# Optimization experiments

Measured on AMD Instinct MI355X. Metric: run time of the kernel, lower is better.

## Reference

```python
import jax, jax.numpy as jnp
import numpy as np

OMEGA = 10.0
SIGMA = 10.0
HID = 256
IN_DIM = 3
OUT_DIM = 3


def gabor(x, W, b):
    # torch.nn.Linear: lin = x @ W.T + b
    lin = x @ W.T + b
    # exp(1j*omega*lin - (sigma*lin)**2).real == cos(omega*lin) * exp(-(sigma*lin)**2)
    return jnp.cos(OMEGA * lin) * jnp.exp(-jnp.square(SIGMA * lin))


def _linear_init(key, out_dim, in_dim):
    kw, kb = jax.random.split(key)
    bound = 1.0 / np.sqrt(in_dim)
    W = jax.random.uniform(kw, (out_dim, in_dim), jnp.float32, -bound, bound)
    b = jax.random.uniform(kb, (out_dim,), jnp.float32, -bound, bound)
    return W, b


def setup_inputs() -> dict:
    key = jax.random.key(0)
    keys = jax.random.split(key, 7)
    N = 262144
    x = jax.random.uniform(keys[0], (N, IN_DIM), jnp.float32)
    W0, b0 = _linear_init(keys[1], HID, IN_DIM)
    W1, b1 = _linear_init(keys[2], HID, HID)
    W2, b2 = _linear_init(keys[3], HID, HID)
    W3, b3 = _linear_init(keys[4], HID, HID + IN_DIM)  # skip-concat layer
    W4, b4 = _linear_init(keys[5], HID, HID)
    Wf, bf = _linear_init(keys[6], OUT_DIM, HID)
    return {"x": x, "W0": W0, "b0": b0, "W1": W1, "b1": b1, "W2": W2,
            "b2": b2, "W3": W3, "b3": b3, "W4": W4, "b4": b4,
            "Wf": Wf, "bf": bf}


def reference(x, W0, b0, W1, b1, W2, b2, W3, b3, W4, b4, Wf, bf):
    x_in = x
    h = gabor(x, W0, b0)          # net[0]
    h = gabor(h, W1, b1)          # net[1]
    h = gabor(h, W2, b2)          # net[2]
    h = jnp.concatenate([h, x_in], axis=-1)  # skip before net[3]
    h = gabor(h, W3, b3)          # net[3]
    h = gabor(h, W4, b4)          # net[4]
    return h @ Wf.T + bf          # final linear
```

## Files before the change

### kernel.cpp

```cpp
#include <hip/hip_runtime.h>

typedef _Float16 f16x8 __attribute__((ext_vector_type(8)));
typedef _Float16 f16x4 __attribute__((ext_vector_type(4)));
typedef float    f32x4 __attribute__((ext_vector_type(4)));

#define BN    64
#define KPAD  288
#define ROWB  (KPAD * 2)
#define WELE  270336

__device__ __forceinline__ int swz(int row, int colb) {
  int c = (colb < 512) ? (colb ^ ((row & 7) << 4)) : colb;
  return row * ROWB + c;
}

__device__ __forceinline__ float gabor_f(float lin) {
  float a = 10.f * lin;
  return __cosf(a) * __expf(-a * a);
}

template <int KS>
__device__ __forceinline__ void mfma_layer(const char* __restrict__ inb,
                                           char* __restrict__ outb,
                                           const _Float16* __restrict__ Wh,
                                           const _Float16* __restrict__ Wl,
                                           const float* __restrict__ bias,
                                           int lane, int wid) {
  const int r = lane & 15;
  const int g = lane >> 4;
  const int n0 = wid * 32;
  const int x = (r & 7) << 4;

  int boff[4][2];
#pragma unroll
  for (int j = 0; j < 4; j++) {
    const int row = j * 16 + r;
    boff[j][0] = row * ROWB + ((g * 16) ^ x);
    boff[j][1] = row * ROWB + ((64 + g * 16) ^ x);
  }

  f32x4 acc[2][4];
#pragma unroll
  for (int i = 0; i < 2; i++)
#pragma unroll
    for (int j = 0; j < 4; j++) {
      f32x4 z = {0.f, 0.f, 0.f, 0.f};
      acc[i][j] = z;
    }

  const int wbase = (wid * KS) * 1024 + lane * 8;

#pragma unroll
  for (int kk = 0; kk < KS; kk++) {
    const int wof = wbase + kk * 1024;
    f16x8 a0 = *(const f16x8*)(Wh + wof);
    f16x8 a1 = *(const f16x8*)(Wh + wof + 512);
    f16x8 c0 = *(const f16x8*)(Wl + wof);
    f16x8 c1 = *(const f16x8*)(Wl + wof + 512);

    f16x8 b0, b1, b2, b3;
    if (kk < 8) {
      const int imm = (kk >> 1) * 128;
      b0 = *(const f16x8*)(inb + boff[0][kk & 1] + imm);
      b1 = *(const f16x8*)(inb + boff[1][kk & 1] + imm);
      b2 = *(const f16x8*)(inb + boff[2][kk & 1] + imm);
      b3 = *(const f16x8*)(inb + boff[3][kk & 1] + imm);
    } else {
      const int lin0 = r * ROWB + 512 + g * 16;
      b0 = *(const f16x8*)(inb + lin0);
      b1 = *(const f16x8*)(inb + lin0 + 16 * ROWB);
      b2 = *(const f16x8*)(inb + lin0 + 32 * ROWB);
      b3 = *(const f16x8*)(inb + lin0 + 48 * ROWB);
    }

    acc[0][0] = __builtin_amdgcn_mfma_f32_16x16x32_f16(a0, b0, acc[0][0], 0, 0, 0);
    acc[0][1] = __builtin_amdgcn_mfma_f32_16x16x32_f16(a0, b1, acc[0][1], 0, 0, 0);
    acc[0][2] = __builtin_amdgcn_mfma_f32_16x16x32_f16(a0, b2, acc[0][2], 0, 0, 0);
    acc[0][3] = __builtin_amdgcn_mfma_f32_16x16x32_f16(a0, b3, acc[0][3], 0, 0, 0);
    acc[1][0] = __builtin_amdgcn_mfma_f32_16x16x32_f16(a1, b0, acc[1][0], 0, 0, 0);
    acc[1][1] = __builtin_amdgcn_mfma_f32_16x16x32_f16(a1, b1, acc[1][1], 0, 0, 0);
    acc[1][2] = __builtin_amdgcn_mfma_f32_16x16x32_f16(a1, b2, acc[1][2], 0, 0, 0);
    acc[1][3] = __builtin_amdgcn_mfma_f32_16x16x32_f16(a1, b3, acc[1][3], 0, 0, 0);
    acc[0][0] = __builtin_amdgcn_mfma_f32_16x16x32_f16(c0, b0, acc[0][0], 0, 0, 0);
    acc[0][1] = __builtin_amdgcn_mfma_f32_16x16x32_f16(c0, b1, acc[0][1], 0, 0, 0);
    acc[0][2] = __builtin_amdgcn_mfma_f32_16x16x32_f16(c0, b2, acc[0][2], 0, 0, 0);
    acc[0][3] = __builtin_amdgcn_mfma_f32_16x16x32_f16(c0, b3, acc[0][3], 0, 0, 0);
    acc[1][0] = __builtin_amdgcn_mfma_f32_16x16x32_f16(c1, b0, acc[1][0], 0, 0, 0);
    acc[1][1] = __builtin_amdgcn_mfma_f32_16x16x32_f16(c1, b1, acc[1][1], 0, 0, 0);
    acc[1][2] = __builtin_amdgcn_mfma_f32_16x16x32_f16(c1, b2, acc[1][2], 0, 0, 0);
    acc[1][3] = __builtin_amdgcn_mfma_f32_16x16x32_f16(c1, b3, acc[1][3], 0, 0, 0);
  }

#pragma unroll
  for (int i = 0; i < 2; i++) {
    const f32x4 bv = *(const f32x4*)(bias + n0 + i * 16 + g * 4);
#pragma unroll
    for (int j = 0; j < 4; j++) {
      f16x4 hv;
#pragma unroll
      for (int e = 0; e < 4; e++)
        hv[e] = (_Float16)gabor_f(acc[i][j][e] + bv[e]);
      *(f16x4*)(outb + swz(j * 16 + r, (n0 + i * 16 + g * 4) * 2)) = hv;
    }
  }
}

extern "C" __global__ void __launch_bounds__(512, 3)
inr_fused(const float* __restrict__ x, const float* __restrict__ W0,
          const float* __restrict__ b0, const float* __restrict__ b1,
          const float* __restrict__ b2, const float* __restrict__ b3,
          const float* __restrict__ b4, const float* __restrict__ Wf,
          const float* __restrict__ bf, const _Float16* __restrict__ wsh,
          float* __restrict__ out, int npts) {
  extern __shared__ char smem[];
  char* bufA = smem;
  char* bufB = smem + BN * ROWB;

  const _Float16* w1h = wsh;
  const _Float16* w2h = wsh + 65536;
  const _Float16* w4h = wsh + 131072;
  const _Float16* w3p = wsh + 196608;
  const _Float16* w1l = wsh + WELE;
  const _Float16* w2l = wsh + WELE + 65536;
  const _Float16* w4l = wsh + WELE + 131072;
  const _Float16* w3l = wsh + WELE + 196608;

  const int tid   = threadIdx.x;
  const int pbase = blockIdx.x * BN;

  {
    const int p = tid >> 3;
    const int q = tid & 7;
    const int gp = pbase + p;
    float x0 = 0.f, x1 = 0.f, x2 = 0.f;
    if (gp < npts) {
      x0 = x[(size_t)gp * 3 + 0];
      x1 = x[(size_t)gp * 3 + 1];
      x2 = x[(size_t)gp * 3 + 2];
    }
#pragma unroll
    for (int ub = 0; ub < 32; ub += 8) {
      const int u0 = q * 32 + ub;
      f16x8 hv;
#pragma unroll
      for (int e = 0; e < 8; e++) {
        const int u = u0 + e;
        float lin = fmaf(x0, W0[u * 3 + 0],
                    fmaf(x1, W0[u * 3 + 1],
                    fmaf(x2, W0[u * 3 + 2], b0[u])));
        hv[e] = (_Float16)gabor_f(lin);
      }
      *(f16x8*)(bufA + swz(p, u0 * 2)) = hv;
    }
    if (q < 4) {
      f16x8 xv = {(_Float16)0.f, (_Float16)0.f, (_Float16)0.f, (_Float16)0.f,
                  (_Float16)0.f, (_Float16)0.f, (_Float16)0.f, (_Float16)0.f};
      if (q == 0) { xv[0] = (_Float16)x0; xv[1] = (_Float16)x1; xv[2] = (_Float16)x2; }
      *(f16x8*)(bufA + swz(p, (256 + q * 8) * 2)) = xv;
    }
  }
  __syncthreads();

  const int lane = tid & 63;
  const int wid  = tid >> 6;

  mfma_layer<8>(bufA, bufB, w1h, w1l, b1, lane, wid);
  __syncthreads();
  mfma_layer<8>(bufB, bufA, w2h, w2l, b2, lane, wid);
  __syncthreads();
  mfma_layer<9>(bufA, bufB, w3p, w3l, b3, lane, wid);
  __syncthreads();
  mfma_layer<8>(bufB, bufA, w4h, w4l, b4, lane, wid);
  __syncthreads();

  {
    const int p = tid >> 3;
    const int q = tid & 7;
    const int gp = pbase + p;
    const int xo = (p & 7) << 4;
    const char* rowp = bufA + p * ROWB;
    float s0 = 0.f, s1 = 0.f, s2 = 0.f;
#pragma unroll
    for (int i8 = 0; i8 < 4; i8++) {
      const int ke = q * 32 + i8 * 8;
      f16x8 hv = *(const f16x8*)(rowp + ((ke * 2) ^ xo));
      const f32x4 w0a = *(const f32x4*)(Wf + 0 * 256 + ke);
      const f32x4 w0b = *(const f32x4*)(Wf + 0 * 256 + ke + 4);
      const f32x4 w1a = *(const f32x4*)(Wf + 1 * 256 + ke);
      const f32x4 w1b = *(const f32x4*)(Wf + 1 * 256 + ke + 4);
      const f32x4 w2a = *(const f32x4*)(Wf + 2 * 256 + ke);
      const f32x4 w2b = *(const f32x4*)(Wf + 2 * 256 + ke + 4);
#pragma unroll
      for (int e = 0; e < 4; e++) {
        const float ha = (float)hv[e];
        const float hb = (float)hv[e + 4];
        s0 = fmaf(ha, w0a[e], fmaf(hb, w0b[e], s0));
        s1 = fmaf(ha, w1a[e], fmaf(hb, w1b[e], s1));
        s2 = fmaf(ha, w2a[e], fmaf(hb, w2b[e], s2));
      }
    }
#pragma unroll
    for (int m = 1; m < 8; m <<= 1) {
      s0 += __shfl_xor(s0, m, 64);
      s1 += __shfl_xor(s1, m, 64);
      s2 += __shfl_xor(s2, m, 64);
    }
    if (gp < npts && q < 3) {
      const float v = (q == 0) ? (s0 + bf[0]) : ((q == 1) ? (s1 + bf[1]) : (s2 + bf[2]));
      out[(size_t)gp * 3 + q] = v;
    }
  }
}

extern "C" __global__ void conv_w(const float* __restrict__ W1,
                                  const float* __restrict__ W2,
                                  const float* __restrict__ W4,
                                  const float* __restrict__ W3,
                                  _Float16* __restrict__ wsh) {
  int idx = blockIdx.x * blockDim.x + threadIdx.x;
  if (idx >= WELE) return;

  int base, KS;
  const float* src = nullptr;
  int ldk = 256, kmax = 256;
  if (idx < 65536)       { base = 0;      KS = 8; src = W1; }
  else if (idx < 131072) { base = 65536;  KS = 8; src = W2; }
  else if (idx < 196608) { base = 131072; KS = 8; src = W4; }
  else                   { base = 196608; KS = 9; src = W3; ldk = 259; kmax = 259; }

  const int t    = idx - base;
  const int e    = t & 7;
  const int lane = (t >> 3) & 63;
  const int i    = (t >> 9) & 1;
  const int rem  = t >> 10;
  const int kk   = rem % KS;
  const int slice = rem / KS;

  const int unit = slice * 32 + i * 16 + (lane & 15);
  const int k    = kk * 32 + (lane >> 4) * 8 + e;

  const float w = (k < kmax) ? src[(size_t)unit * ldk + k] : 0.f;
  const _Float16 hi = (_Float16)w;
  const _Float16 lo = (_Float16)(w - (float)hi);
  wsh[idx] = hi;
  wsh[idx + WELE] = lo;
}

extern "C" void kernel_launch(void* const* d_in, const int* in_sizes, int n_in,
                              void* d_out, int out_size, void* d_ws, size_t ws_size,
                              hipStream_t stream) {
  const float* x  = (const float*)d_in[0];
  const float* W0 = (const float*)d_in[1];
  const float* b0 = (const float*)d_in[2];
  const float* W1 = (const float*)d_in[3];
  const float* b1 = (const float*)d_in[4];
  const float* W2 = (const float*)d_in[5];
  const float* b2 = (const float*)d_in[6];
  const float* W3 = (const float*)d_in[7];
  const float* b3 = (const float*)d_in[8];
  const float* W4 = (const float*)d_in[9];
  const float* b4 = (const float*)d_in[10];
  const float* Wf = (const float*)d_in[11];
  const float* bf = (const float*)d_in[12];
  float* out      = (float*)d_out;
  _Float16* wsh   = (_Float16*)d_ws;

  const int npts = in_sizes[0] / 3;

  conv_w<<<(WELE + 511) / 512, 512, 0, stream>>>(W1, W2, W4, W3, wsh);

  const int nblk = (npts + BN - 1) / BN;
  inr_fused<<<nblk, 512, 2 * BN * ROWB, stream>>>(x, W0, b0, b1, b2, b3, b4,
                                                  Wf, bf, wsh, out, npts);
}
```

Before: 415.3 us.

## Double-buffer weight loads with manual waitcnt and rotate per-block K order

Each layer's per-k-step global weight fragment loads are now issued one step ahead into a double buffer using inline-asm global loads, with explicit vmcnt waits. This overlaps weight fetch latency with the MFMA work and the LDS activation reads. Each block starts its K loop at a different offset (blockIdx & 7) so concurrent blocks spread their weight reads. Biases are staged in LDS, and launch bounds drop to 2 waves-per-EU, giving the extra buffered registers room. The manual waitcnt relies on no other global loads being in flight inside the loop, and the relaxed bound may change register allocation and occupancy.

```diff
diff --git a/kernel.cpp b/kernel.cpp
--- a/kernel.cpp
+++ b/kernel.cpp
@@ -1,4 +1,5 @@
 #include <hip/hip_runtime.h>
+#include <stdint.h>
 
 typedef _Float16 f16x8 __attribute__((ext_vector_type(8)));
 typedef _Float16 f16x4 __attribute__((ext_vector_type(4)));
@@ -8,6 +9,8 @@
 #define KPAD  288
 #define ROWB  (KPAD * 2)
 #define WELE  270336
+#define LDS_ACT (2 * BN * ROWB)
+#define LDS_TOTAL (LDS_ACT + 4096)
 
 __device__ __forceinline__ int swz(int row, int colb) {
   int c = (colb < 512) ? (colb ^ ((row & 7) << 4)) : colb;
@@ -17,6 +20,25 @@
 __device__ __forceinline__ float gabor_f(float lin) {
   float a = 10.f * lin;
   return __cosf(a) * __expf(-a * a);
+}
+
+struct WSet { f32x4 h0, h1, l0, l1; };
+
+#define GLOADX4(dst, p)                                                  \
+  asm volatile("global_load_dwordx4 %0, %1, off"                         \
+               : "=v"(dst) : "v"((uint64_t)(uintptr_t)(p)))
+
+#define WAITW4(s) asm volatile("s_waitcnt vmcnt(4)"                      \
+  : "+v"((s).h0), "+v"((s).h1), "+v"((s).l0), "+v"((s).l1))
+#define WAITW0(s) asm volatile("s_waitcnt vmcnt(0)"                      \
+  : "+v"((s).h0), "+v"((s).h1), "+v"((s).l0), "+v"((s).l1))
+
+__device__ __forceinline__ void issueW(WSet& s, const _Float16* Wh,
+                                       const _Float16* Wl, int wof) {
+  GLOADX4(s.h0, Wh + wof);
+  GLOADX4(s.h1, Wh + wof + 512);
+  GLOADX4(s.l0, Wl + wof);
+  GLOADX4(s.l1, Wl + wof + 512);
 }
 
 template <int KS>
@@ -24,21 +46,11 @@
                                            char* __restrict__ outb,
                                            const _Float16* __restrict__ Wh,
                                            const _Float16* __restrict__ Wl,
-                                           const float* __restrict__ bias,
-                                           int lane, int wid) {
+                                           const float* __restrict__ lbias,
+                                           int lane, int wid, int phase) {
   const int r = lane & 15;
   const int g = lane >> 4;
   const int n0 = wid * 32;
-  const int x = (r & 7) << 4;
-
-  int boff[4][2];
-#pragma unroll
-  for (int j = 0; j < 4; j++) {
-    const int row = j * 16 + r;
-    boff[j][0] = row * ROWB + ((g * 16) ^ x);
-    boff[j][1] = row * ROWB + ((64 + g * 16) ^ x);
-  }
-
   f32x4 acc[2][4];
 #pragma unroll
   for (int i = 0; i < 2; i++)
@@ -48,52 +60,63 @@
       acc[i][j] = z;
     }
 
-  const int wbase = (wid * KS) * 1024 + lane * 8;
+  const int wbase = wid * KS * 1024 + lane * 8;
+
+  WSet w[2];
+  {
+    const int kkr = phase;
+    issueW(w[0], Wh, Wl, wbase + kkr * 1024);
+  }
 
 #pragma unroll
   for (int kk = 0; kk < KS; kk++) {
-    const int wof = wbase + kk * 1024;
-    f16x8 a0 = *(const f16x8*)(Wh + wof);
-    f16x8 a1 = *(const f16x8*)(Wh + wof + 512);
-    f16x8 c0 = *(const f16x8*)(Wl + wof);
-    f16x8 c1 = *(const f16x8*)(Wl + wof + 512);
-
-    f16x8 b0, b1, b2, b3;
-    if (kk < 8) {
-      const int imm = (kk >> 1) * 128;
-      b0 = *(const f16x8*)(inb + boff[0][kk & 1] + imm);
-      b1 = *(const f16x8*)(inb + boff[1][kk & 1] + imm);
-      b2 = *(const f16x8*)(inb + boff[2][kk & 1] + imm);
-      b3 = *(const f16x8*)(inb + boff[3][kk & 1] + imm);
-    } else {
-      const int lin0 = r * ROWB + 512 + g * 16;
-      b0 = *(const f16x8*)(inb + lin0);
-      b1 = *(const f16x8*)(inb + lin0 + 16 * ROWB);
-      b2 = *(const f16x8*)(inb + lin0 + 32 * ROWB);
-      b3 = *(const f16x8*)(inb + lin0 + 48 * ROWB);
-    }
-
-    acc[0][0] = __builtin_amdgcn_mfma_f32_16x16x32_f16(a0, b0, acc[0][0], 0, 0, 0);
-    acc[0][1] = __builtin_amdgcn_mfma_f32_16x16x32_f16(a0, b1, acc[0][1], 0, 0, 0);
-    acc[0][2] = __builtin_amdgcn_mfma_f32_16x16x32_f16(a0, b2, acc[0][2], 0, 0, 0);
-    acc[0][3] = __builtin_amdgcn_mfma_f32_16x16x32_f16(a0, b3, acc[0][3], 0, 0, 0);
-    acc[1][0] = __builtin_amdgcn_mfma_f32_16x16x32_f16(a1, b0, acc[1][0], 0, 0, 0);
-    acc[1][1] = __builtin_amdgcn_mfma_f32_16x16x32_f16(a1, b1, acc[1][1], 0, 0, 0);
-    acc[1][2] = __builtin_amdgcn_mfma_f32_16x16x32_f16(a1, b2, acc[1][2], 0, 0, 0);
-    acc[1][3] = __builtin_amdgcn_mfma_f32_16x16x32_f16(a1, b3, acc[1][3], 0, 0, 0);
-    acc[0][0] = __builtin_amdgcn_mfma_f32_16x16x32_f16(c0, b0, acc[0][0], 0, 0, 0);
-    acc[0][1] = __builtin_amdgcn_mfma_f32_16x16x32_f16(c0, b1, acc[0][1], 0, 0, 0);
-    acc[0][2] = __builtin_amdgcn_mfma_f32_16x16x32_f16(c0, b2, acc[0][2], 0, 0, 0);
-    acc[0][3] = __builtin_amdgcn_mfma_f32_16x16x32_f16(c0, b3, acc[0][3], 0, 0, 0);
-    acc[1][0] = __builtin_amdgcn_mfma_f32_16x16x32_f16(c1, b0, acc[1][0], 0, 0, 0);
-    acc[1][1] = __builtin_amdgcn_mfma_f32_16x16x32_f16(c1, b1, acc[1][1], 0, 0, 0);
-    acc[1][2] = __builtin_amdgcn_mfma_f32_16x16x32_f16(c1, b2, acc[1][2], 0, 0, 0);
-    acc[1][3] = __builtin_amdgcn_mfma_f32_16x16x32_f16(c1, b3, acc[1][3], 0, 0, 0);
+    const int cur = kk & 1;
+    const int nxt = cur ^ 1;
+
+    int kkr = kk + phase;
+    if (kkr >= KS) kkr -= KS;
+
+    const bool haveNext = (kk + 1 < KS);
+    if (haveNext) {
+      int kkn = kk + 1 + phase;
+      if (kkn >= KS) kkn -= KS;
+      issueW(w[nxt], Wh, Wl, wbase + kkn * 1024);
+    }
+
+    const int kb = kkr * 32 + g * 8;
+    f16x8 b0 = *(const f16x8*)(inb + swz(0 * 16 + r, kb * 2));
+    f16x8 b1 = *(const f16x8*)(inb + swz(1 * 16 + r, kb * 2));
+    f16x8 b2 = *(const f16x8*)(inb + swz(2 * 16 + r, kb * 2));
+    f16x8 b3 = *(const f16x8*)(inb + swz(3 * 16 + r, kb * 2));
+
+    if (haveNext) WAITW4(w[cur]); else WAITW0(w[cur]);
+
+    const f16x8 ah0 = __builtin_bit_cast(f16x8, w[cur].h0);
+    const f16x8 ah1 = __builtin_bit_cast(f16x8, w[cur].h1);
+    const f16x8 al0 = __builtin_bit_cast(f16x8, w[cur].l0);
+    const f16x8 al1 = __builtin_bit_cast(f16x8, w[cur].l1);
+
+    acc[0][0] = __builtin_amdgcn_mfma_f32_16x16x32_f16(ah0, b0, acc[0][0], 0, 0, 0);
+    acc[0][1] = __builtin_amdgcn_mfma_f32_16x16x32_f16(ah0, b1, acc[0][1], 0, 0, 0);
+    acc[0][2] = __builtin_amdgcn_mfma_f32_16x16x32_f16(ah0, b2, acc[0][2], 0, 0, 0);
+    acc[0][3] = __builtin_amdgcn_mfma_f32_16x16x32_f16(ah0, b3, acc[0][3], 0, 0, 0);
+    acc[1][0] = __builtin_amdgcn_mfma_f32_16x16x32_f16(ah1, b0, acc[1][0], 0, 0, 0);
+    acc[1][1] = __builtin_amdgcn_mfma_f32_16x16x32_f16(ah1, b1, acc[1][1], 0, 0, 0);
+    acc[1][2] = __builtin_amdgcn_mfma_f32_16x16x32_f16(ah1, b2, acc[1][2], 0, 0, 0);
+    acc[1][3] = __builtin_amdgcn_mfma_f32_16x16x32_f16(ah1, b3, acc[1][3], 0, 0, 0);
+    acc[0][0] = __builtin_amdgcn_mfma_f32_16x16x32_f16(al0, b0, acc[0][0], 0, 0, 0);
+    acc[0][1] = __builtin_amdgcn_mfma_f32_16x16x32_f16(al0, b1, acc[0][1], 0, 0, 0);
+    acc[0][2] = __builtin_amdgcn_mfma_f32_16x16x32_f16(al0, b2, acc[0][2], 0, 0, 0);
+    acc[0][3] = __builtin_amdgcn_mfma_f32_16x16x32_f16(al0, b3, acc[0][3], 0, 0, 0);
+    acc[1][0] = __builtin_amdgcn_mfma_f32_16x16x32_f16(al1, b0, acc[1][0], 0, 0, 0);
+    acc[1][1] = __builtin_amdgcn_mfma_f32_16x16x32_f16(al1, b1, acc[1][1], 0, 0, 0);
+    acc[1][2] = __builtin_amdgcn_mfma_f32_16x16x32_f16(al1, b2, acc[1][2], 0, 0, 0);
+    acc[1][3] = __builtin_amdgcn_mfma_f32_16x16x32_f16(al1, b3, acc[1][3], 0, 0, 0);
   }
 
 #pragma unroll
   for (int i = 0; i < 2; i++) {
-    const f32x4 bv = *(const f32x4*)(bias + n0 + i * 16 + g * 4);
+    const f32x4 bv = *(const f32x4*)(lbias + n0 + i * 16 + g * 4);
 #pragma unroll
     for (int j = 0; j < 4; j++) {
       f16x4 hv;
@@ -105,7 +128,7 @@
   }
 }
 
-extern "C" __global__ void __launch_bounds__(512, 3)
+extern "C" __global__ void __launch_bounds__(512, 2)
 inr_fused(const float* __restrict__ x, const float* __restrict__ W0,
           const float* __restrict__ b0, const float* __restrict__ b1,
           const float* __restrict__ b2, const float* __restrict__ b3,
@@ -115,6 +138,7 @@
   extern __shared__ char smem[];
   char* bufA = smem;
   char* bufB = smem + BN * ROWB;
+  float* lbias = (float*)(smem + LDS_ACT);
 
   const _Float16* w1h = wsh;
   const _Float16* w2h = wsh + 65536;
@@ -127,6 +151,14 @@
 
   const int tid   = threadIdx.x;
   const int pbase = blockIdx.x * BN;
+  const int phase = blockIdx.x & 7;
+
+  if (tid < 256) {
+    lbias[tid]       = b1[tid];
+    lbias[256 + tid] = b2[tid];
+    lbias[512 + tid] = b3[tid];
+    lbias[768 + tid] = b4[tid];
+  }
 
   {
     const int p = tid >> 3;
@@ -164,14 +196,15 @@
   const int lane = tid & 63;
   const int wid  = tid >> 6;
 
-  mfma_layer<8>(bufA, bufB, w1h, w1l, b1, lane, wid);
-  __syncthreads();
-  mfma_layer<8>(bufB, bufA, w2h, w2l, b2, lane, wid);
-  __syncthreads();
-  mfma_layer<9>(bufA, bufB, w3p, w3l, b3, lane, wid);
-  __syncthreads();
-  mfma_layer<8>(bufB, bufA, w4h, w4l, b4, lane, wid);
-  __syncthreads();
+  mfma_layer<8>(bufA, bufB, w1h, w1l, lbias,       lane, wid, phase);
+  __syncthreads();
+  mfma_layer<8>(bufB, bufA, w2h, w2l, lbias + 256, lane, wid, phase);
+  __syncthreads();
+  mfma_layer<9>(bufA, bufB, w3p, w3l, lbias + 512, lane, wid, phase);
+  __syncthreads();
+  mfma_layer<8>(bufB, bufA, w4h, w4l, lbias + 768, lane, wid, phase);
+  __syncthreads();
+  __builtin_amdgcn_sched_barrier(0);
 
   {
     const int p = tid >> 3;
@@ -270,6 +303,6 @@
   conv_w<<<(WELE + 511) / 512, 512, 0, stream>>>(W1, W2, W4, W3, wsh);
 
   const int nblk = (npts + BN - 1) / BN;
-  inr_fused<<<nblk, 512, 2 * BN * ROWB, stream>>>(x, W0, b0, b1, b2, b3, b4,
-                                                  Wf, bf, wsh, out, npts);
-}
+  inr_fused<<<nblk, 512, LDS_TOTAL, stream>>>(x, W0, b0, b1, b2, b3, b4,
+                                              Wf, bf, wsh, out, npts);
+}
```

Measured after the change: 486.8 us. 17.2% more time.
